# Kernel tuning notes

Hardware: AMD Instinct MI355X
Metric: run time of the kernel (lower is better)

Reference implementation:

```python
import jax, jax.numpy as jnp
import numpy as np

B, L, D = 4, 4096, 1024
H = 16
BS = 64                      # block_size
HD = D // H                  # head_dim = 64
NB = L // BS                 # num_blocks = 64 (L multiple of BS -> no padding)
SCALE = HD ** -0.5
TEMP = 0.7
N_SINK_ITERS = 7


def setup_inputs() -> dict:
    key = jax.random.key(0)
    ks = jax.random.split(key, 7)
    x = jax.random.normal(ks[0], (B, L, D), dtype=jnp.float32)
    # gumbel noise matching torch.rand_like(log_alpha) -> -log(-log(u+eps)+eps)
    u = jax.random.uniform(ks[1], (B, H, NB, NB), dtype=jnp.float32)
    gumbel = -jnp.log(-jnp.log(u + 1e-20) + 1e-20)
    s_in = 1.0 / np.sqrt(D)
    W_qkv = jax.random.normal(ks[2], (D, 3 * D), dtype=jnp.float32) * s_in
    b_qkv = jnp.zeros((3 * D,), dtype=jnp.float32)
    W_out = jax.random.normal(ks[3], (D, D), dtype=jnp.float32) * s_in
    b_out = jnp.zeros((D,), dtype=jnp.float32)
    return {"x": x, "gumbel": gumbel, "W_qkv": W_qkv, "b_qkv": b_qkv,
            "W_out": W_out, "b_out": b_out}


def _sinkhorn(log_alpha):
    # Gumbel noise already added by caller; iterate row/col log-normalization.
    for _ in range(N_SINK_ITERS):
        log_alpha = log_alpha - jax.nn.logsumexp(log_alpha, axis=-1, keepdims=True)
        log_alpha = log_alpha - jax.nn.logsumexp(log_alpha, axis=-2, keepdims=True)
    return jnp.exp(log_alpha)


def reference(x, gumbel, W_qkv, b_qkv, W_out, b_out):
    qkv = x @ W_qkv + b_qkv                              # [B,L,3D]
    q, k, v = jnp.split(qkv, 3, axis=-1)

    def to_blocks(t):  # [B,L,D] -> [B,H,NB,BS,HD]
        return t.reshape(B, L, H, HD).transpose(0, 2, 1, 3).reshape(B, H, NB, BS, HD)

    q_b, k_b, v_b = to_blocks(q), to_blocks(k), to_blocks(v)

    # block summaries and Gumbel-Sinkhorn permutation over blocks
    q_repr = q_b.mean(axis=3)                            # [B,H,NB,HD]
    k_repr = k_b.mean(axis=3)
    sim = jnp.einsum('bhnd,bhmd->bhnm', q_repr, k_repr) * SCALE
    P = _sinkhorn((sim + gumbel) / TEMP)                 # [B,H,NB,NB]

    # sort K/V blocks via soft permutation
    k_flat = k_b.reshape(B, H, NB, BS * HD)
    v_flat = v_b.reshape(B, H, NB, BS * HD)
    k_sorted = jnp.einsum('bhnm,bhmf->bhnf', P, k_flat).reshape(B, H, NB, BS, HD)
    v_sorted = jnp.einsum('bhnm,bhmf->bhnf', P, v_flat).reshape(B, H, NB, BS, HD)

    # block i attends to [own block, sorted block i+1]; last block only to itself
    k_next = jnp.roll(k_sorted, -1, axis=2)
    v_next = jnp.roll(v_sorted, -1, axis=2)
    k_local = jnp.concatenate([k_b, k_next], axis=3)     # [B,H,NB,2BS,HD]
    v_local = jnp.concatenate([v_b, v_next], axis=3)

    scores = jnp.einsum('bhnqd,bhnkd->bhnqk', q_b, k_local) * SCALE
    # mask second half of keys for last block (it only attends to itself)
    scores = scores.at[:, :, -1, :, BS:].set(-1e9)
    attn = jax.nn.softmax(scores, axis=-1)               # dropout: eval -> identity
    out = jnp.einsum('bhnqk,bhnkd->bhnqd', attn, v_local)

    out = out.reshape(B, H, L, HD).transpose(0, 2, 1, 3).reshape(B, L, D)
    return out @ W_out + b_out
```

## Files before the change

kernel.cpp:

```cpp
#include <hip/hip_runtime.h>
#include <cstdint>
#include <cstddef>
#include <cstdio>

#define B_   4
#define L_   4096
#define D_   1024
#define H_   16
#define BS_  64
#define HD_  64
#define NB_  64
#define SCALE_   0.125f
#define INV_TEMP (1.0f/0.7f)

typedef unsigned short bf16_t;

#ifndef __has_builtin
#define __has_builtin(x) 0
#endif
#if __has_builtin(__builtin_amdgcn_global_load_lds)
#define HAS_GLD 1
#else
#define HAS_GLD 0
#endif

#if HAS_GLD
#define GLD16(gp, lp) __builtin_amdgcn_global_load_lds(                        \
    (__attribute__((address_space(1))) void*)(uintptr_t)(gp),                  \
    (__attribute__((address_space(3))) void*)(unsigned int)(uintptr_t)(lp),    \
    16, 0, 0)
#endif

__device__ __forceinline__ float b2f(bf16_t u) {
    union { unsigned int i; float f; } c; c.i = ((unsigned int)u) << 16; return c.f;
}
__device__ __forceinline__ bf16_t f2b(float f) {
    union { float f; unsigned int i; } c; c.f = f;
    unsigned int r = c.i + 0x7FFFu + ((c.i >> 16) & 1u);
    return (bf16_t)(r >> 16);
}

__device__ __forceinline__ void storeC(float* p, float v)  { *p = v; }
__device__ __forceinline__ void storeC(bf16_t* p, float v) { *p = f2b(v); }

using bf16x8 = __attribute__((ext_vector_type(8))) short;
using f32x4  = __attribute__((ext_vector_type(4))) float;

__global__ __launch_bounds__(256) void f32_to_bf16_kernel(
    const float* __restrict__ src, bf16_t* __restrict__ dst, int n4)
{
    const int i = blockIdx.x * 256 + threadIdx.x;
    if (i < n4) {
        float4 v = *(const float4*)(src + (size_t)i * 4);
        ushort4 o = {f2b(v.x), f2b(v.y), f2b(v.z), f2b(v.w)};
        *(ushort4*)(dst + (size_t)i * 4) = o;
    }
}

__global__ __launch_bounds__(256) void transpose_f32_bf16_kernel(
    const float* __restrict__ src, bf16_t* __restrict__ dst, int R, int C)
{
    __shared__ float t[32][33];
    const int c0 = blockIdx.x * 32, r0 = blockIdx.y * 32;
    for (int i = threadIdx.y; i < 32; i += 8)
        t[i][threadIdx.x] = src[(size_t)(r0 + i) * C + c0 + threadIdx.x];
    __syncthreads();
    for (int i = threadIdx.y; i < 32; i += 8)
        dst[(size_t)(c0 + i) * R + r0 + threadIdx.x] = f2b(t[threadIdx.x][i]);
}

#if HAS_GLD
#define SGA(tt, hb, dst)                                                       \
    GLD16(gAb + (size_t)((hb) * 128) * K + (size_t)(tt) * 64,                  \
          (dst) + (((hb) * 128 + w * 16) * 64));                               \
    GLD16(gAb + (size_t)((hb) * 128 + 8) * K + (size_t)(tt) * 64,              \
          (dst) + (((hb) * 128 + w * 16 + 8) * 64))
#define SGB(tt, hb, dst)                                                       \
    GLD16(gBb + (size_t)((hb) * 128) * K + (size_t)(tt) * 64,                  \
          (dst) + (((hb) * 128 + w * 16) * 64));                               \
    GLD16(gBb + (size_t)((hb) * 128 + 8) * K + (size_t)(tt) * 64,              \
          (dst) + (((hb) * 128 + w * 16 + 8) * 64))
#else
#define SGA(tt, hb, dst)                                                       \
    *(bf16x8*)((dst) + (((hb) * 128 + w * 16) * 64) + lane * 8) =              \
        *(const bf16x8*)(gAb + (size_t)((hb) * 128) * K + (size_t)(tt) * 64);  \
    *(bf16x8*)((dst) + (((hb) * 128 + w * 16 + 8) * 64) + lane * 8) =          \
        *(const bf16x8*)(gAb + (size_t)((hb) * 128 + 8) * K + (size_t)(tt) * 64)
#define SGB(tt, hb, dst)                                                       \
    *(bf16x8*)((dst) + (((hb) * 128 + w * 16) * 64) + lane * 8) =              \
        *(const bf16x8*)(gBb + (size_t)((hb) * 128) * K + (size_t)(tt) * 64);  \
    *(bf16x8*)((dst) + (((hb) * 128 + w * 16 + 8) * 64) + lane * 8) =          \
        *(const bf16x8*)(gBb + (size_t)((hb) * 128 + 8) * K + (size_t)(tt) * 64)
#endif

#define PHASE(ABUF, p, STAGE, ENDWAIT)                                         \
  {                                                                            \
    bf16x8 a0k0 = *(const bf16x8*)&(ABUF)[aRow0 + (2*(p))   * 1024 + csw[0]];  \
    bf16x8 a0k1 = *(const bf16x8*)&(ABUF)[aRow0 + (2*(p))   * 1024 + csw[1]];  \
    bf16x8 a1k0 = *(const bf16x8*)&(ABUF)[aRow0 + (2*(p)+1) * 1024 + csw[0]];  \
    bf16x8 a1k1 = *(const bf16x8*)&(ABUF)[aRow0 + (2*(p)+1) * 1024 + csw[1]];  \
    STAGE;                                                                     \
    __builtin_amdgcn_s_barrier();                                              \
    asm volatile("s_waitcnt lgkmcnt(0)" ::: "memory");                         \
    __builtin_amdgcn_s_setprio(1);                                             \
    _Pragma("unroll")                                                          \
    for (int fn = 0; fn < 4; ++fn) {                                           \
      acc[2*(p)][fn]   = __builtin_amdgcn_mfma_f32_16x16x32_bf16(              \
          a0k0, bq[fn][0], acc[2*(p)][fn], 0, 0, 0);                           \
      acc[2*(p)][fn]   = __builtin_amdgcn_mfma_f32_16x16x32_bf16(              \
          a0k1, bq[fn][1], acc[2*(p)][fn], 0, 0, 0);                           \
      acc[2*(p)+1][fn] = __builtin_amdgcn_mfma_f32_16x16x32_bf16(              \
          a1k0, bq[fn][0], acc[2*(p)+1][fn], 0, 0, 0);                         \
      acc[2*(p)+1][fn] = __builtin_amdgcn_mfma_f32_16x16x32_bf16(              \
          a1k1, bq[fn][1], acc[2*(p)+1][fn], 0, 0, 0);                         \
    }                                                                          \
    __builtin_amdgcn_s_setprio(0);                                             \
    ENDWAIT;                                                                   \
    __builtin_amdgcn_s_barrier();                                              \
    asm volatile("" ::: "memory");                                             \
  }

#define KTILE(ABUF, BBUF, NABUF, t)                                            \
  {                                                                            \
    bf16x8 bq[4][2];                                                           \
    _Pragma("unroll")                                                          \
    for (int fn = 0; fn < 4; ++fn) {                                           \
      bq[fn][0] = *(const bf16x8*)&(BBUF)[bRow0 + fn * 1024 + csw[0]];         \
      bq[fn][1] = *(const bf16x8*)&(BBUF)[bRow0 + fn * 1024 + csw[1]];         \
    }                                                                          \
    const bool stA = ((t) + 1 < KT), stB = ((t) + 2 < KT);                     \
    PHASE(ABUF, 0, if (stA) { SGA((t) + 1, 0, NABUF); }, )                     \
    PHASE(ABUF, 1, if (stA) { SGA((t) + 1, 1, NABUF); }, )                     \
    PHASE(ABUF, 2, if (stB) { SGB((t) + 2, 0, BBUF); }, )                      \
    PHASE(ABUF, 3, if (stB) { SGB((t) + 2, 1, BBUF); },                        \
          if ((t) + 1 < KT) {                                                  \
            if (stB) { asm volatile("s_waitcnt vmcnt(4)" ::: "memory"); }      \
            else     { asm volatile("s_waitcnt vmcnt(0)" ::: "memory"); }      \
          })                                                                   \
  }

template<typename TC>
__global__ __launch_bounds__(512, 2) void gemm256_8phase_kernel(
    const bf16_t* __restrict__ A, const bf16_t* __restrict__ Bt,
    const float* __restrict__ bias, TC* __restrict__ C,
    int M, int N, int K)
{
    __shared__ __align__(16) short sm[65536];
    short* const smA0 = sm;
    short* const smB0 = sm + 16384;
    short* const smA1 = sm + 32768;
    short* const smB1 = sm + 49152;

    const int tid  = threadIdx.x;
    const int lane = tid & 63;
    const int w    = tid >> 6;
    const int wr   = w >> 2, wc = w & 3;
    const int ml   = lane & 15, q2 = lane >> 4;
    const int m0   = blockIdx.y * 256, n0 = blockIdx.x * 256;
    const int KT   = K >> 6;

    int csw[2];
    csw[0] = ((q2)     ^ (ml & 7)) * 8;
    csw[1] = ((4 + q2) ^ (ml & 7)) * 8;
    const int aRow0 = (wr * 128 + ml) * 64;
    const int bRow0 = (wc * 64  + ml) * 64;

    const int rl   = lane >> 3;
    const int scol = ((lane & 7) ^ rl) * 8;
    const bf16_t* gAb = A  + (size_t)(m0 + w * 16 + rl) * K + scol;
    const bf16_t* gBb = Bt + (size_t)(n0 + w * 16 + rl) * K + scol;

    f32x4 acc[8][4];
    #pragma unroll
    for (int i = 0; i < 8; ++i)
        #pragma unroll
        for (int j = 0; j < 4; ++j)
            acc[i][j] = {0.f, 0.f, 0.f, 0.f};

    SGA(0, 0, smA0); SGA(0, 1, smA0);
    SGB(0, 0, smB0); SGB(0, 1, smB0);
    SGB(1, 0, smB1); SGB(1, 1, smB1);
    asm volatile("s_waitcnt vmcnt(4)" ::: "memory");
    __builtin_amdgcn_s_barrier();
    asm volatile("" ::: "memory");

    for (int t = 0; t < KT; t += 2) {
        KTILE(smA0, smB0, smA1, t);
        KTILE(smA1, smB1, smA0, t + 1);
    }

    float bv[4];
    #pragma unroll
    for (int fn = 0; fn < 4; ++fn)
        bv[fn] = bias[n0 + wc * 64 + fn * 16 + ml];
    #pragma unroll
    for (int fm = 0; fm < 8; ++fm)
        #pragma unroll
        for (int fn = 0; fn < 4; ++fn)
            #pragma unroll
            for (int r = 0; r < 4; ++r) {
                const int row = m0 + wr * 128 + fm * 16 + q2 * 4 + r;
                const int col = n0 + wc * 64  + fn * 16 + ml;
                storeC(&C[(size_t)row * N + col], acc[fm][fn][r] + bv[fn]);
            }
}

#undef KTILE
#undef PHASE
#undef SGA
#undef SGB

__global__ __launch_bounds__(64) void block_repr_kernel(
    const bf16_t* __restrict__ qkv,
    float* __restrict__ q_repr, float* __restrict__ k_repr)
{
    const int blk = blockIdx.x;
    const int n  = blk & 63;
    const int bh = blk >> 6;
    const int h  = bh & 15, b = bh >> 4;
    const int d  = threadIdx.x;
    const bf16_t* base = qkv + (size_t)(b * L_ + n * BS_) * (3 * D_) + h * HD_ + d;
    float sq = 0.f, sk = 0.f;
    for (int s = 0; s < BS_; ++s) {
        sq += b2f(base[(size_t)s * (3 * D_)]);
        sk += b2f(base[(size_t)s * (3 * D_) + D_]);
    }
    q_repr[(size_t)blk * HD_ + d] = sq * (1.0f / BS_);
    k_repr[(size_t)blk * HD_ + d] = sk * (1.0f / BS_);
}

__global__ __launch_bounds__(64) void sinkhorn_kernel(
    const float* __restrict__ q_repr, const float* __restrict__ k_repr,
    const float* __restrict__ gumbel, bf16_t* __restrict__ P_bf)
{
    __shared__ float qr[64][65];
    __shared__ float kr[64][65];
    __shared__ float la[64][65];
    const int bh = blockIdx.x;
    const int t  = threadIdx.x;

    for (int i = 0; i < 64; ++i) {
        qr[i][t] = q_repr[((size_t)bh * 64 + i) * 64 + t];
        kr[i][t] = k_repr[((size_t)bh * 64 + i) * 64 + t];
    }
    __syncthreads();

    for (int m = 0; m < 64; ++m) {
        float s = 0.f;
        for (int d = 0; d < 64; ++d) s += qr[t][d] * kr[m][d];
        la[t][m] = (s * SCALE_ + gumbel[((size_t)bh * 64 + t) * 64 + m]) * INV_TEMP;
    }
    __syncthreads();

    for (int it = 0; it < 7; ++it) {
        {
            float mx = -1e30f;
            for (int m = 0; m < 64; ++m) mx = fmaxf(mx, la[t][m]);
            float sum = 0.f;
            for (int m = 0; m < 64; ++m) sum += expf(la[t][m] - mx);
            const float lse = mx + logf(sum);
            for (int m = 0; m < 64; ++m) la[t][m] -= lse;
        }
        __syncthreads();
        {
            float mx = -1e30f;
            for (int m = 0; m < 64; ++m) mx = fmaxf(mx, la[m][t]);
            float sum = 0.f;
            for (int m = 0; m < 64; ++m) sum += expf(la[m][t] - mx);
            const float lse = mx + logf(sum);
            for (int m = 0; m < 64; ++m) la[m][t] -= lse;
        }
        __syncthreads();
    }

    for (int i = 0; i < 64; ++i)
        P_bf[((size_t)bh * 64 + i) * 64 + t] = f2b(expf(la[i][t]));
}

__global__ __launch_bounds__(256) void sort_kv_mfma_kernel(
    const bf16_t* __restrict__ P_bf, const bf16_t* __restrict__ qkv,
    bf16_t* __restrict__ k_sorted, bf16_t* __restrict__ v_sorted)
{
    constexpr int TS = 72;
    __shared__ short Pl[64 * TS];
    const int tid = threadIdx.x, lane = tid & 63, w = tid >> 6;
    const int bh = blockIdx.y;
    const int h = bh & 15, b = bh >> 4;
    const int c = blockIdx.x;
    const int ml = lane & 15, q8 = (lane >> 4) * 8;

    {
        const int r = tid >> 3, cc = (tid & 7) * 8;
        const bf16_t* ps = P_bf + (size_t)bh * (NB_ * NB_);
        *(bf16x8*)&Pl[r * TS + cc]        = *(const bf16x8*)&ps[r * 64 + cc];
        *(bf16x8*)&Pl[(r + 32) * TS + cc] = *(const bf16x8*)&ps[(r + 32) * 64 + cc];
    }
    __syncthreads();

    const int s = c * 4 + w;
    const int fbase = c * 256 + w * 64;

    for (int kv = 0; kv < 2; ++kv) {
        const bf16_t* src = qkv + ((size_t)(b * L_ + s)) * (3 * D_)
                          + (kv ? 2 * D_ : 1 * D_) + h * HD_;
        bf16x8 bt[4][2];
        #pragma unroll
        for (int t = 0; t < 4; ++t)
            #pragma unroll
            for (int kt = 0; kt < 2; ++kt)
                #pragma unroll
                for (int j = 0; j < 8; ++j)
                    bt[t][kt][j] = (short)src[
                        (size_t)(kt * 32 + q8 + j) * (BS_ * 3 * D_) + t * 16 + ml];

        f32x4 acc[4][4];
        #pragma unroll
        for (int nt = 0; nt < 4; ++nt)
            #pragma unroll
            for (int t = 0; t < 4; ++t)
                acc[nt][t] = {0.f, 0.f, 0.f, 0.f};

        #pragma unroll
        for (int nt = 0; nt < 4; ++nt) {
            bf16x8 a0 = *(const bf16x8*)&Pl[(nt * 16 + ml) * TS + q8];
            bf16x8 a1 = *(const bf16x8*)&Pl[(nt * 16 + ml) * TS + 32 + q8];
            #pragma unroll
            for (int t = 0; t < 4; ++t) {
                acc[nt][t] = __builtin_amdgcn_mfma_f32_16x16x32_bf16(
                    a0, bt[t][0], acc[nt][t], 0, 0, 0);
                acc[nt][t] = __builtin_amdgcn_mfma_f32_16x16x32_bf16(
                    a1, bt[t][1], acc[nt][t], 0, 0, 0);
            }
        }

        bf16_t* dst = (kv ? v_sorted : k_sorted) + (size_t)bh * (NB_ * BS_ * HD_);
        const int quad4 = (lane >> 4) * 4;
        #pragma unroll
        for (int nt = 0; nt < 4; ++nt)
            #pragma unroll
            for (int t = 0; t < 4; ++t)
                #pragma unroll
                for (int r = 0; r < 4; ++r)
                    dst[(size_t)(nt * 16 + quad4 + r) * (BS_ * HD_)
                        + fbase + t * 16 + ml] = f2b(acc[nt][t][r]);
    }
}

__global__ __launch_bounds__(256) void attn_mfma_kernel(
    const bf16_t* __restrict__ qkv, const bf16_t* __restrict__ k_sorted,
    const bf16_t* __restrict__ v_sorted, bf16_t* __restrict__ attn_out)
{
    constexpr int KS = 72, VS = 136, PS = 136;
    __shared__ short Ks[128 * KS];
    __shared__ short Vt[64 * VS];
    __shared__ short Psh[64 * PS];
    const int tid = threadIdx.x, lane = tid & 63, w = tid >> 6;
    const int n  = blockIdx.x & 63;
    const int bh = blockIdx.x >> 6;
    const int h = bh & 15, b = bh >> 4;
    const bool last = (n == NB_ - 1);

    const bf16_t* qb = qkv + (size_t)(b * L_ + n * BS_) * (3 * D_) + h * HD_;
    const bf16_t* kb = qb + D_;
    const bf16_t* vb = qb + 2 * D_;
    const size_t nextoff = ((size_t)bh * NB_ + (n + 1)) * (size_t)(BS_ * HD_);
    const bf16_t* kn = k_sorted + nextoff;
    const bf16_t* vn = v_sorted + nextoff;

    {
        const int col8 = (tid & 7) * 8, r0 = tid >> 3;
        const int jjmax = last ? 2 : 4;
        for (int jj = 0; jj < jjmax; ++jj) {
            const int row = jj * 32 + r0;
            const bf16_t* src = (row < 64)
                ? kb + (size_t)row * (3 * D_) + col8
                : kn + (size_t)(row - 64) * HD_ + col8;
            *(bf16x8*)&Ks[row * KS + col8] = *(const bf16x8*)src;
        }
    }
    {
        const int halves = last ? 1 : 2;
        for (int half = 0; half < halves; ++half) {
            for (int jj = 0; jj < 4; ++jj) {
                const int d0 = jj * 16 + w * 4;
                const bf16_t* src = (half == 0)
                    ? vb + (size_t)lane * (3 * D_) + d0
                    : vn + (size_t)lane * HD_ + d0;
                ushort4 u = *(const ushort4*)src;
                const int kcol = half * 64 + lane;
                Vt[(d0 + 0) * VS + kcol] = u.x;
                Vt[(d0 + 1) * VS + kcol] = u.y;
                Vt[(d0 + 2) * VS + kcol] = u.z;
                Vt[(d0 + 3) * VS + kcol] = u.w;
            }
        }
    }

    const int ml = lane & 15, quad = lane >> 4, q8 = quad * 8;
    const int m0 = w * 16;

    bf16x8 af0 = *(const bf16x8*)(qb + (size_t)(m0 + ml) * (3 * D_) + q8);
    bf16x8 af1 = *(const bf16x8*)(qb + (size_t)(m0 + ml) * (3 * D_) + 32 + q8);

    __syncthreads();

    const int ntile = last ? 4 : 8;
    f32x4 st[8];
    #pragma unroll
    for (int t = 0; t < 8; ++t) st[t] = {0.f, 0.f, 0.f, 0.f};
    for (int t = 0; t < ntile; ++t) {
        bf16x8 b0 = *(const bf16x8*)&Ks[(t * 16 + ml) * KS + q8];
        bf16x8 b1 = *(const bf16x8*)&Ks[(t * 16 + ml) * KS + 32 + q8];
        st[t] = __builtin_amdgcn_mfma_f32_16x16x32_bf16(af0, b0, st[t], 0, 0, 0);
        st[t] = __builtin_amdgcn_mfma_f32_16x16x32_bf16(af1, b1, st[t], 0, 0, 0);
    }

    #pragma unroll
    for (int reg = 0; reg < 4; ++reg) {
        float mx = -1e30f;
        for (int t = 0; t < ntile; ++t) mx = fmaxf(mx, st[t][reg] * SCALE_);
        #pragma unroll
        for (int xm = 1; xm <= 8; xm <<= 1)
            mx = fmaxf(mx, __shfl_xor(mx, xm, 64));
        float e[8];
        float sum = 0.f;
        for (int t = 0; t < ntile; ++t) {
            e[t] = __expf(st[t][reg] * SCALE_ - mx);
            sum += e[t];
        }
        #pragma unroll
        for (int xm = 1; xm <= 8; xm <<= 1)
            sum += __shfl_xor(sum, xm, 64);
        const float inv = 1.0f / sum;
        const int qrow = m0 + quad * 4 + reg;
        for (int t = 0; t < ntile; ++t)
            Psh[qrow * PS + t * 16 + ml] = f2b(e[t] * inv);
    }

    __syncthreads();

    const int ktv = last ? 2 : 4;
    f32x4 oacc[4];
    #pragma unroll
    for (int t = 0; t < 4; ++t) oacc[t] = {0.f, 0.f, 0.f, 0.f};
    for (int kt = 0; kt < ktv; ++kt) {
        bf16x8 pa = *(const bf16x8*)&Psh[(m0 + ml) * PS + kt * 32 + q8];
        #pragma unroll
        for (int t = 0; t < 4; ++t) {
            bf16x8 vf = *(const bf16x8*)&Vt[(t * 16 + ml) * VS + kt * 32 + q8];
            oacc[t] = __builtin_amdgcn_mfma_f32_16x16x32_bf16(pa, vf, oacc[t], 0, 0, 0);
        }
    }

    bf16_t* ob = attn_out + (size_t)(b * L_ + n * BS_) * D_ + h * HD_;
    #pragma unroll
    for (int t = 0; t < 4; ++t)
        #pragma unroll
        for (int reg = 0; reg < 4; ++reg) {
            const int qrow = m0 + quad * 4 + reg;
            ob[(size_t)qrow * D_ + t * 16 + ml] = f2b(oacc[t][reg]);
        }
}

extern "C" void kernel_launch(void* const* d_in, const int* in_sizes, int n_in,
                              void* d_out, int out_size, void* d_ws, size_t ws_size,
                              hipStream_t stream)
{
    const float* x      = (const float*)d_in[0];
    const float* gumbel = (const float*)d_in[1];
    const float* W_qkv  = (const float*)d_in[2];
    const float* b_qkv  = (const float*)d_in[3];
    const float* W_out  = (const float*)d_in[4];
    const float* b_out  = (const float*)d_in[5];
    float* out = (float*)d_out;

    const size_t need = 204472320ull;
    if (ws_size < need) {
        fprintf(stderr, "[kernel_launch] ws_size=%zu < need=%zu — aborting launch\n",
                ws_size, need);
        return;
    }

    bf16_t* qkv      = (bf16_t*)d_ws;
    bf16_t* attn_o   = qkv    + (size_t)B_ * L_ * 3 * D_;
    bf16_t* k_sorted = attn_o + (size_t)B_ * L_ * D_;
    bf16_t* v_sorted = k_sorted + (size_t)B_ * L_ * D_;
    float* q_repr    = (float*)(v_sorted + (size_t)B_ * L_ * D_);
    float* k_repr    = q_repr + (size_t)B_ * H_ * NB_ * HD_;
    bf16_t* P_bf     = (bf16_t*)(k_repr + (size_t)B_ * H_ * NB_ * HD_);

    bf16_t* x_bf   = (bf16_t*)d_out;
    bf16_t* Wqkv_t = x_bf + (size_t)B_ * L_ * D_;
    bf16_t* Wout_t = (bf16_t*)q_repr;

    f32_to_bf16_kernel<<<(B_ * L_ * D_ / 4 + 255) / 256, 256, 0, stream>>>(
        x, x_bf, B_ * L_ * D_ / 4);
    transpose_f32_bf16_kernel<<<dim3(3 * D_ / 32, D_ / 32), dim3(32, 8), 0, stream>>>(
        W_qkv, Wqkv_t, D_, 3 * D_);

    gemm256_8phase_kernel<bf16_t>
        <<<dim3(3 * D_ / 256, B_ * L_ / 256), 512, 0, stream>>>(
        x_bf, Wqkv_t, b_qkv, qkv, B_ * L_, 3 * D_, D_);

    block_repr_kernel<<<B_ * H_ * NB_, 64, 0, stream>>>(qkv, q_repr, k_repr);

    sinkhorn_kernel<<<B_ * H_, 64, 0, stream>>>(q_repr, k_repr, gumbel, P_bf);

    sort_kv_mfma_kernel<<<dim3(16, B_ * H_), 256, 0, stream>>>(
        P_bf, qkv, k_sorted, v_sorted);

    attn_mfma_kernel<<<B_ * H_ * NB_, 256, 0, stream>>>(
        qkv, k_sorted, v_sorted, attn_o);

    transpose_f32_bf16_kernel<<<dim3(D_ / 32, D_ / 32), dim3(32, 8), 0, stream>>>(
        W_out, Wout_t, D_, D_);

    gemm256_8phase_kernel<float>
        <<<dim3(D_ / 256, B_ * L_ / 256), 512, 0, stream>>>(
        attn_o, Wout_t, b_out, out, B_ * L_, D_, D_);
}
```

Before: 487.3 us.

## Parallelize sinkhorn and block_repr across 256 threads, swizzle GEMM tile order

Sinkhorn now uses 256 threads per (b,h): four threads per row with a register-tiled float4 dot product, and the row and column logsumexps are reduced with lane shuffles. block_repr splits the 64-row sum across four warps and combines them in shared memory. The GEMM remaps workgroup IDs in groups of eight, aimed at better L2 or cross-XCD locality. The sort_kv gather loop is also reordered so loads from the same row are adjacent. The aim is to remove the serial, low-occupancy cost of the single-wave sinkhorn and repr kernels, at the price of extra syncs and more register use.

Result: faster. 417.3 us (-14.4%).

```diff
diff --git a/kernel.cpp b/kernel.cpp
--- a/kernel.cpp
+++ b/kernel.cpp
@@ -156,7 +156,14 @@
     const int w    = tid >> 6;
     const int wr   = w >> 2, wc = w & 3;
     const int ml   = lane & 15, q2 = lane >> 4;
-    const int m0   = blockIdx.y * 256, n0 = blockIdx.x * 256;
+
+    const int gx  = gridDim.x;
+    const int nwg = gx * gridDim.y;
+    const int bid = blockIdx.y * gx + blockIdx.x;
+    int swz = bid;
+    if ((nwg & 7) == 0) swz = (bid & 7) * (nwg >> 3) + (bid >> 3);
+    const int m0 = (swz / gx) * 256, n0 = (swz % gx) * 256;
+
     const int KT   = K >> 6;
 
     int csw[2];
@@ -210,71 +217,126 @@
 #undef SGA
 #undef SGB
 
-__global__ __launch_bounds__(64) void block_repr_kernel(
+__global__ __launch_bounds__(256) void block_repr_kernel(
     const bf16_t* __restrict__ qkv,
     float* __restrict__ q_repr, float* __restrict__ k_repr)
 {
+    __shared__ float red[2][4][64];
     const int blk = blockIdx.x;
     const int n  = blk & 63;
     const int bh = blk >> 6;
     const int h  = bh & 15, b = bh >> 4;
-    const int d  = threadIdx.x;
+    const int d  = threadIdx.x & 63;
+    const int ss = threadIdx.x >> 6;
     const bf16_t* base = qkv + (size_t)(b * L_ + n * BS_) * (3 * D_) + h * HD_ + d;
     float sq = 0.f, sk = 0.f;
-    for (int s = 0; s < BS_; ++s) {
+    for (int s = ss; s < BS_; s += 4) {
         sq += b2f(base[(size_t)s * (3 * D_)]);
         sk += b2f(base[(size_t)s * (3 * D_) + D_]);
     }
-    q_repr[(size_t)blk * HD_ + d] = sq * (1.0f / BS_);
-    k_repr[(size_t)blk * HD_ + d] = sk * (1.0f / BS_);
-}
-
-__global__ __launch_bounds__(64) void sinkhorn_kernel(
+    red[0][ss][d] = sq;
+    red[1][ss][d] = sk;
+    __syncthreads();
+    if (threadIdx.x < 64) {
+        const int dd = threadIdx.x;
+        q_repr[(size_t)blk * HD_ + dd] =
+            (red[0][0][dd] + red[0][1][dd] + red[0][2][dd] + red[0][3][dd])
+            * (1.0f / BS_);
+    } else if (threadIdx.x < 128) {
+        const int dd = threadIdx.x - 64;
+        k_repr[(size_t)blk * HD_ + dd] =
+            (red[1][0][dd] + red[1][1][dd] + red[1][2][dd] + red[1][3][dd])
+            * (1.0f / BS_);
+    }
+}
+
+__global__ __launch_bounds__(256) void sinkhorn_kernel(
     const float* __restrict__ q_repr, const float* __restrict__ k_repr,
     const float* __restrict__ gumbel, bf16_t* __restrict__ P_bf)
 {
-    __shared__ float qr[64][65];
-    __shared__ float kr[64][65];
-    __shared__ float la[64][65];
-    const int bh = blockIdx.x;
-    const int t  = threadIdx.x;
-
-    for (int i = 0; i < 64; ++i) {
-        qr[i][t] = q_repr[((size_t)bh * 64 + i) * 64 + t];
-        kr[i][t] = k_repr[((size_t)bh * 64 + i) * 64 + t];
-    }
-    __syncthreads();
-
-    for (int m = 0; m < 64; ++m) {
-        float s = 0.f;
-        for (int d = 0; d < 64; ++d) s += qr[t][d] * kr[m][d];
-        la[t][m] = (s * SCALE_ + gumbel[((size_t)bh * 64 + t) * 64 + m]) * INV_TEMP;
+    __shared__ __align__(16) float qr[64 * 68];
+    __shared__ __align__(16) float kr[64 * 68];
+    __shared__ float la[64 * 65];
+    const int bh  = blockIdx.x;
+    const int tid = threadIdx.x;
+    const int r   = tid >> 2;
+    const int sub = tid & 3;
+
+    for (int idx = tid; idx < 4096; idx += 256) {
+        const int rr = idx >> 6, cc = idx & 63;
+        qr[rr * 68 + cc] = q_repr[(size_t)bh * 4096 + idx];
+        kr[rr * 68 + cc] = k_repr[(size_t)bh * 4096 + idx];
+    }
+    __syncthreads();
+
+    {
+        float acc[16];
+        #pragma unroll
+        for (int mi = 0; mi < 16; ++mi) acc[mi] = 0.f;
+        for (int d4 = 0; d4 < 16; ++d4) {
+            const float4 q = *(const float4*)&qr[r * 68 + d4 * 4];
+            #pragma unroll
+            for (int mi = 0; mi < 16; ++mi) {
+                const float4 kv = *(const float4*)&kr[(4 * mi + sub) * 68 + d4 * 4];
+                acc[mi] += q.x * kv.x + q.y * kv.y + q.z * kv.z + q.w * kv.w;
+            }
+        }
+        #pragma unroll
+        for (int mi = 0; mi < 16; ++mi) {
+            const int m = 4 * mi + sub;
+            la[r * 65 + m] = (acc[mi] * SCALE_
+                + gumbel[(size_t)bh * 4096 + r * 64 + m]) * INV_TEMP;
+        }
     }
     __syncthreads();
 
     for (int it = 0; it < 7; ++it) {
         {
-            float mx = -1e30f;
-            for (int m = 0; m < 64; ++m) mx = fmaxf(mx, la[t][m]);
+            float v[16];
+            #pragma unroll
+            for (int mi = 0; mi < 16; ++mi) v[mi] = la[r * 65 + 4 * mi + sub];
+            float mx = v[0];
+            #pragma unroll
+            for (int mi = 1; mi < 16; ++mi) mx = fmaxf(mx, v[mi]);
+            mx = fmaxf(mx, __shfl_xor(mx, 1, 64));
+            mx = fmaxf(mx, __shfl_xor(mx, 2, 64));
             float sum = 0.f;
-            for (int m = 0; m < 64; ++m) sum += expf(la[t][m] - mx);
+            #pragma unroll
+            for (int mi = 0; mi < 16; ++mi) sum += expf(v[mi] - mx);
+            sum += __shfl_xor(sum, 1, 64);
+            sum += __shfl_xor(sum, 2, 64);
             const float lse = mx + logf(sum);
-            for (int m = 0; m < 64; ++m) la[t][m] -= lse;
+            #pragma unroll
+            for (int mi = 0; mi < 16; ++mi) la[r * 65 + 4 * mi + sub] = v[mi] - lse;
         }
         __syncthreads();
         {
-            float mx = -1e30f;
-            for (int m = 0; m < 64; ++m) mx = fmaxf(mx, la[m][t]);
+            float v[16];
+            #pragma unroll
+            for (int mi = 0; mi < 16; ++mi) v[mi] = la[(4 * mi + sub) * 65 + r];
+            float mx = v[0];
+            #pragma unroll
+            for (int mi = 1; mi < 16; ++mi) mx = fmaxf(mx, v[mi]);
+            mx = fmaxf(mx, __shfl_xor(mx, 1, 64));
+            mx = fmaxf(mx, __shfl_xor(mx, 2, 64));
             float sum = 0.f;
-            for (int m = 0; m < 64; ++m) sum += expf(la[m][t] - mx);
+            #pragma unroll
+            for (int mi = 0; mi < 16; ++mi) sum += expf(v[mi] - mx);
+            sum += __shfl_xor(sum, 1, 64);
+            sum += __shfl_xor(sum, 2, 64);
             const float lse = mx + logf(sum);
-            for (int m = 0; m < 64; ++m) la[m][t] -= lse;
+            #pragma unroll
+            for (int mi = 0; mi < 16; ++mi)
+                la[(4 * mi + sub) * 65 + r] = v[mi] - lse;
         }
         __syncthreads();
     }
 
-    for (int i = 0; i < 64; ++i)
-        P_bf[((size_t)bh * 64 + i) * 64 + t] = f2b(expf(la[i][t]));
+    #pragma unroll
+    for (int mi = 0; mi < 16; ++mi) {
+        const int m = 4 * mi + sub;
+        P_bf[(size_t)bh * 4096 + r * 64 + m] = f2b(expf(la[r * 65 + m]));
+    }
 }
 
 __global__ __launch_bounds__(256) void sort_kv_mfma_kernel(
@@ -305,13 +367,15 @@
                           + (kv ? 2 * D_ : 1 * D_) + h * HD_;
         bf16x8 bt[4][2];
         #pragma unroll
-        for (int t = 0; t < 4; ++t)
-            #pragma unroll
-            for (int kt = 0; kt < 2; ++kt)
+        for (int kt = 0; kt < 2; ++kt)
+            #pragma unroll
+            for (int j = 0; j < 8; ++j) {
+                const bf16_t* rp = src
+                    + (size_t)(kt * 32 + q8 + j) * (BS_ * 3 * D_) + ml;
                 #pragma unroll
-                for (int j = 0; j < 8; ++j)
-                    bt[t][kt][j] = (short)src[
-                        (size_t)(kt * 32 + q8 + j) * (BS_ * 3 * D_) + t * 16 + ml];
+                for (int t = 0; t < 4; ++t)
+                    bt[t][kt][j] = (short)rp[t * 16];
+            }
 
         f32x4 acc[4][4];
         #pragma unroll
@@ -502,9 +566,9 @@
         <<<dim3(3 * D_ / 256, B_ * L_ / 256), 512, 0, stream>>>(
         x_bf, Wqkv_t, b_qkv, qkv, B_ * L_, 3 * D_, D_);
 
-    block_repr_kernel<<<B_ * H_ * NB_, 64, 0, stream>>>(qkv, q_repr, k_repr);
-
-    sinkhorn_kernel<<<B_ * H_, 64, 0, stream>>>(q_repr, k_repr, gumbel, P_bf);
+    block_repr_kernel<<<B_ * H_ * NB_, 256, 0, stream>>>(qkv, q_repr, k_repr);
+
+    sinkhorn_kernel<<<B_ * H_, 256, 0, stream>>>(q_repr, k_repr, gumbel, P_bf);
 
     sort_kv_mfma_kernel<<<dim3(16, B_ * H_), 256, 0, stream>>>(
         P_bf, qkv, k_sorted, v_sorted);
```
